# Optimization experiments

Measured on AMD Instinct MI355X. Metric: run time of the kernel, lower is better.

Reference implementation:

```python
import jax, jax.numpy as jnp
import numpy as np

B, N = 32, 200000          # images, flattened candidates per image (anchors*classes)
NUM_CLASSES = 21           # VOC-style class count for the label-offset trick
CONF_THR = 0.05            # cfg.PRED_CONF_THR
NMS_THR = 0.5              # cfg.PRED_NMS_THR
TOPK = 500                 # cfg.PRED_SELECT_TOPK
KEEP_MAX = 100             # cfg.PRED_NMS_KEEP


def setup_inputs() -> dict:
    key = jax.random.key(0)
    k1, k2, k3, k4 = jax.random.split(key, 4)
    pscores = jax.random.uniform(k1, (B, N), dtype=jnp.float32)
    # well-formed ltrb boxes in [0,1]: right>left, bottom>top
    xy1 = jax.random.uniform(k2, (B, N, 2), dtype=jnp.float32) * 0.8
    wh = jax.random.uniform(k3, (B, N, 2), dtype=jnp.float32) * 0.2 + 0.01
    pboxes = jnp.concatenate([xy1, xy1 + wh], axis=-1)
    plabels = jax.random.randint(k4, (B, N), 0, NUM_CLASSES)
    return {"pscores": pscores, "pboxes": pboxes, "plabels": plabels}


def _box_iou(a, b):
    # a: [K,4], b: [K,4] ltrb -> [K,K] pairwise IoU (torchvision convention)
    lt = jnp.maximum(a[:, None, :2], b[None, :, :2])
    rb = jnp.minimum(a[:, None, 2:], b[None, :, 2:])
    wh = jnp.clip(rb - lt, 0.0)
    inter = wh[..., 0] * wh[..., 1]
    area_a = (a[:, 2] - a[:, 0]) * (a[:, 3] - a[:, 1])
    area_b = (b[:, 2] - b[:, 0]) * (b[:, 3] - b[:, 1])
    return inter / (area_a[:, None] + area_b[None, :] - inter)


def _greedy_nms(iou_mat, valid, thr):
    # candidates are pre-sorted by score descending (lax.top_k output order)
    K = valid.shape[0]
    idxs = jnp.arange(K)

    def body(keep, i):
        suppressed = jnp.any(keep & (iou_mat[i] > thr) & (idxs < i))
        k = valid[i] & (~suppressed)
        return keep.at[i].set(k), None

    keep, _ = jax.lax.scan(body, jnp.zeros((K,), dtype=bool), idxs)
    return keep


def reference(pscores, pboxes, plabels):
    # ---- threshold + top-k pre-selection (mask_pos AND mask_topk) ----
    scores_k, idx = jax.lax.top_k(pscores, TOPK)          # [B,K] sorted desc
    valid = scores_k > CONF_THR                           # equivalent to mask_pos & mask_topk
    bidx = jnp.arange(B)[:, None]
    boxes_k = pboxes[bidx, idx]                           # [B,K,4]
    labels_k = plabels[bidx, idx]                         # [B,K]

    # ---- multi-class NMS via label offset trick (batched_nms) ----
    max_coord = jnp.max(jnp.where(valid[..., None], boxes_k, 0.0), axis=(1, 2))  # [B]
    offsets = labels_k.astype(boxes_k.dtype) * (max_coord[:, None] + 1.0)
    boxes_nms = boxes_k + offsets[..., None]              # [B,K,4]

    iou = jax.vmap(_box_iou)(boxes_nms, boxes_nms)        # [B,K,K]
    keep = jax.vmap(lambda m, v: _greedy_nms(m, v, NMS_THR))(iou, valid)  # [B,K] bool

    # ---- keep[:num_max] per batch ----
    rank = jnp.cumsum(keep.astype(jnp.int32), axis=1)
    keep = keep & (rank <= KEEP_MAX)

    # compact kept entries to front (jnp.argsort is stable -> score order preserved), pad to KEEP_MAX
    order = jnp.argsort(jnp.where(keep, 0, 1), axis=1)[:, :KEEP_MAX]       # [B,KEEP]
    out_valid = jnp.take_along_axis(keep, order, axis=1)                    # [B,KEEP]
    boxes2 = jnp.take_along_axis(boxes_k, order[..., None], axis=1) * out_valid[..., None]
    scores2 = jnp.take_along_axis(scores_k, order, axis=1) * out_valid
    labels2 = jnp.where(out_valid, jnp.take_along_axis(labels_k, order, axis=1), -1)
    ids_batch2 = jnp.where(out_valid, jnp.arange(B)[:, None], -1)
    return ids_batch2, boxes2, labels2, scores2, out_valid
```

## Files before the change

kernel.cpp:

```cpp
#include <hip/hip_runtime.h>
#include <stdint.h>

#pragma clang fp contract(off)

#define BB 32
#define NN 200000
#define N4 50000
#define KK 500
#define KEEPN 100
#define CAND_CAP 4096
#define CONF 0.05f
#define NMSTHR 0.5f
#define CNT_STRIDE 16
#define HBINS 16384
#define HSHIFT 18

typedef unsigned long long u64;


__device__ __forceinline__ unsigned int ordkey(float s) {
    unsigned int u = __float_as_uint(s);
    return (u & 0x80000000u) ? ~u : (u | 0x80000000u);
}

__global__ __launch_bounds__(512) void hist_kernel(const float4* __restrict__ ps4,
                                                   unsigned int* __restrict__ hist) {
    __shared__ unsigned int lh[HBINS];
    const int t = threadIdx.x;
    for (int i = t; i < HBINS; i += 512) lh[i] = 0;
    __syncthreads();
    const int b = blockIdx.y;
    const float4* p = ps4 + (size_t)b * N4;
    for (int i = blockIdx.x * 512 + t; i < N4; i += 8 * 512) {
        float4 v = p[i];
        atomicAdd(&lh[ordkey(v.x) >> HSHIFT], 1u);
        atomicAdd(&lh[ordkey(v.y) >> HSHIFT], 1u);
        atomicAdd(&lh[ordkey(v.z) >> HSHIFT], 1u);
        atomicAdd(&lh[ordkey(v.w) >> HSHIFT], 1u);
    }
    __syncthreads();
    unsigned int* hb = hist + (size_t)b * HBINS;
    for (int i = t; i < HBINS; i += 512) {
        unsigned int s = lh[i];
        if (s) atomicAdd(&hb[i], s);
    }
}

__global__ __launch_bounds__(1024) void scan_kernel(const unsigned int* __restrict__ hist,
                                                    unsigned int* __restrict__ p14arr,
                                                    unsigned int* __restrict__ cnt) {
    __shared__ unsigned int partial[1024];
    const int t = threadIdx.x, b = blockIdx.x;
    if (t == 0) cnt[b * CNT_STRIDE] = 0;
    const unsigned int* hb = hist + (size_t)b * HBINS;
    unsigned int v[16];
    unsigned int tot = 0;
    for (int j = 0; j < 16; ++j) { v[j] = hb[t * 16 + j]; tot += v[j]; }
    partial[t] = tot;
    __syncthreads();
    for (int d = 1; d < 1024; d <<= 1) {
        unsigned int add = (t + d < 1024) ? partial[t + d] : 0u;
        __syncthreads();
        partial[t] += add;
        __syncthreads();
    }
    unsigned int after = (t < 1023) ? partial[t + 1] : 0u;
    unsigned int sn = after;
    for (int j = 15; j >= 0; --j) {
        unsigned int s = sn + v[j];
        if (s >= (unsigned)KK && sn < (unsigned)KK) p14arr[b] = (unsigned)(t * 16 + j);
        sn = s;
    }
}

__global__ __launch_bounds__(256) void compact_kernel(const float4* __restrict__ ps4,
                                                      const unsigned int* __restrict__ p14arr,
                                                      u64* __restrict__ cand,
                                                      unsigned int* __restrict__ cnt) {
    __shared__ u64 sl[2048];
    __shared__ int lcnt;
    __shared__ unsigned int lbase;
    const int t = threadIdx.x;
    if (t == 0) lcnt = 0;
    __syncthreads();
    const int b = blockIdx.y;
    const unsigned int p14 = p14arr[b];
    const float4* p = ps4 + (size_t)b * N4;
    for (int k = 0; k < 2; ++k) {
        int i4 = blockIdx.x * 512 + k * 256 + t;
        if (i4 < N4) {
            float4 v = p[i4];
            int n = i4 << 2;
            unsigned int u;
            u = ordkey(v.x);
            if ((u >> HSHIFT) >= p14) { int pos = atomicAdd(&lcnt, 1);
                sl[pos] = ((u64)u << 32) | (unsigned int)(~(unsigned int)(n)); }
            u = ordkey(v.y);
            if ((u >> HSHIFT) >= p14) { int pos = atomicAdd(&lcnt, 1);
                sl[pos] = ((u64)u << 32) | (unsigned int)(~(unsigned int)(n + 1)); }
            u = ordkey(v.z);
            if ((u >> HSHIFT) >= p14) { int pos = atomicAdd(&lcnt, 1);
                sl[pos] = ((u64)u << 32) | (unsigned int)(~(unsigned int)(n + 2)); }
            u = ordkey(v.w);
            if ((u >> HSHIFT) >= p14) { int pos = atomicAdd(&lcnt, 1);
                sl[pos] = ((u64)u << 32) | (unsigned int)(~(unsigned int)(n + 3)); }
        }
    }
    __syncthreads();
    if (t == 0 && lcnt > 0) lbase = atomicAdd(&cnt[b * CNT_STRIDE], (unsigned)lcnt);
    __syncthreads();
    for (int i = t; i < lcnt; i += 256) {
        unsigned int pos = lbase + (unsigned)i;
        if (pos < CAND_CAP) cand[(size_t)b * CAND_CAP + pos] = sl[i];
    }
}

__global__ __launch_bounds__(1024) void final_kernel(const float* __restrict__ pboxes,
                                                     const int* __restrict__ plabels,
                                                     const u64* __restrict__ cand,
                                                     const unsigned int* __restrict__ cnt,
                                                     float* __restrict__ out) {
    __shared__ u64 kbuf[CAND_CAP];
    __shared__ u64 sel[1024];
    __shared__ float sboxes[KK][4];
    __shared__ float sshift[KK][4];
    __shared__ float sscore[KK];
    __shared__ int slabel[KK];
    __shared__ unsigned int h[256];
    __shared__ int clist[KK];
    __shared__ int ccnt[21], coff[22], cfill[21];
    __shared__ u64 validw[8];
    __shared__ int kept[KEEPN];
    __shared__ float wred[16];
    __shared__ u64 s_prefix;
    __shared__ unsigned int s_bin, s_region, s_cntgt;
    __shared__ int s_sc, s_nk;
    __shared__ float s_maxc;

    const int b = blockIdx.x;
    const int tid = threadIdx.x;
    const int lane = tid & 63;

    int m = (int)cnt[b * CNT_STRIDE];
    if (m > CAND_CAP) m = CAND_CAP;

    for (int i = tid; i < m; i += 1024)
        kbuf[i] = cand[(size_t)b * CAND_CAP + i];
    __syncthreads();

    u64 thr; int seln;
    if (m <= 1024) {
        thr = 0ULL; seln = m;
    } else {
        if (tid == 0) { s_prefix = 0ULL; s_cntgt = 0u; }
        __syncthreads();
        int shift = 56;
        for (; shift >= 0; shift -= 8) {
            if (tid < 256) h[tid] = 0u;
            __syncthreads();
            u64 pref = s_prefix;
            unsigned int cg = s_cntgt;
            for (int i = tid; i < m; i += 1024) {
                u64 k = kbuf[i];
                bool match = (shift == 56) || ((k >> (shift + 8)) == pref);
                if (match) atomicAdd(&h[(unsigned int)((k >> shift) & 0xFF)], 1u);
            }
            __syncthreads();
            for (int d = 1; d < 256; d <<= 1) {
                unsigned int add = (tid < 256 && tid + d < 256) ? h[tid + d] : 0u;
                __syncthreads();
                if (tid < 256) h[tid] += add;
                __syncthreads();
            }
            unsigned int target = (unsigned)KK - cg;
            if (tid < 256) {
                unsigned int st = h[tid];
                unsigned int stn = (tid < 255) ? h[tid + 1] : 0u;
                if (st >= target && stn < target) s_bin = (unsigned)tid;
            }
            __syncthreads();
            if (tid == 0) {
                unsigned int bin = s_bin;
                unsigned int sfx1 = (bin < 255) ? h[bin + 1] : 0u;
                s_region = h[bin] - sfx1;
                s_cntgt = cg + sfx1;
                s_prefix = (shift == 56) ? (u64)bin : ((pref << 8) | (u64)bin);
            }
            __syncthreads();
            if (s_cntgt + s_region <= 1024u) break;
        }
        thr = s_prefix << shift;
        seln = (int)(s_cntgt + s_region);
    }

    if (tid == 0) s_sc = 0;
    __syncthreads();
    for (int r = 0; r < 4; ++r) {
        int i = tid + r * 1024;
        u64 k = (i < m) ? kbuf[i] : 0ULL;
        bool p = (i < m) && (k >= thr);
        u64 mb = __ballot(p);
        int pre = __popcll(mb & ((1ULL << lane) - 1ULL));
        int tot = __popcll(mb);
        int base = 0;
        if (lane == 0 && tot > 0) base = atomicAdd(&s_sc, tot);
        base = __shfl(base, 0);
        if (p) sel[base + pre] = k;
    }
    __syncthreads();

    u64 myk = 0ULL; int myr = 0x7FFFFFFF;
    if (tid < seln) {
        myk = sel[tid];
        int r = 0;
        for (int j = 0; j < seln; ++j) r += (sel[j] > myk) ? 1 : 0;
        myr = r;
    }
    __syncthreads();
    if (tid < seln && myr < KK) sel[myr] = myk;
    __syncthreads();

    float sc = -1.0f;
    if (tid < KK) {
        u64 key = sel[tid];
        unsigned int lo = (unsigned int)key;
        unsigned int hi = (unsigned int)(key >> 32);
        int idx = (int)(~lo);
        unsigned int bits = (hi & 0x80000000u) ? (hi & 0x7FFFFFFFu) : ~hi;
        sc = __uint_as_float(bits);
        sscore[tid] = sc;
        const float4 bx = *(const float4*)(pboxes + (((size_t)b * NN + (size_t)idx) << 2));
        sboxes[tid][0] = bx.x; sboxes[tid][1] = bx.y;
        sboxes[tid][2] = bx.z; sboxes[tid][3] = bx.w;
        slabel[tid] = plabels[(size_t)b * NN + idx];
    }
    __syncthreads();

    bool v = (tid < KK) && (sc > CONF);
    u64 bm = __ballot(v);
    if (lane == 0 && (tid >> 6) < 8) validw[tid >> 6] = bm;
    float lm = 0.0f;
    if (v) lm = fmaxf(fmaxf(sboxes[tid][0], sboxes[tid][1]),
                      fmaxf(sboxes[tid][2], sboxes[tid][3]));
    for (int off = 32; off > 0; off >>= 1) lm = fmaxf(lm, __shfl_down(lm, off));
    if (lane == 0) wred[tid >> 6] = lm;
    __syncthreads();
    if (tid < 64) {
        float x = (tid < 16) ? wred[tid] : 0.0f;
        for (int off = 8; off > 0; off >>= 1) x = fmaxf(x, __shfl_down(x, off));
        if (tid == 0) s_maxc = x;
    }
    __syncthreads();

    if (tid < KK) {
        float off = (float)slabel[tid] * (s_maxc + 1.0f);
        sshift[tid][0] = sboxes[tid][0] + off;
        sshift[tid][1] = sboxes[tid][1] + off;
        sshift[tid][2] = sboxes[tid][2] + off;
        sshift[tid][3] = sboxes[tid][3] + off;
    }
    if (tid < 21) { ccnt[tid] = 0; cfill[tid] = 0; }
    __syncthreads();
    if (tid < KK) atomicAdd(&ccnt[slabel[tid]], 1);
    __syncthreads();
    if (tid == 0) {
        int acc = 0;
        for (int c = 0; c < 21; ++c) { coff[c] = acc; acc += ccnt[c]; }
        coff[21] = acc;
    }
    __syncthreads();
    if (tid < KK) {
        int c = slabel[tid];
        int pos = atomicAdd(&cfill[c], 1);
        clist[coff[c] + pos] = tid;
    }
    for (int i = tid; i < KK * 8; i += 1024) kbuf[i] = 0ULL;
    __syncthreads();

    if (tid < KK) {
        int c = slabel[tid];
        int n = ccnt[c], base = coff[c];
        float a0 = sshift[tid][0], a1 = sshift[tid][1],
              a2 = sshift[tid][2], a3 = sshift[tid][3];
        float areaA = (a2 - a0) * (a3 - a1);
        for (int q = 0; q < n; ++q) {
            int j = clist[base + q];
            float b0 = sshift[j][0], b1f = sshift[j][1],
                  b2f = sshift[j][2], b3f = sshift[j][3];
            float lt0 = fmaxf(a0, b0), lt1 = fmaxf(a1, b1f);
            float rb0 = fminf(a2, b2f), rb1 = fminf(a3, b3f);
            float ww = fmaxf(rb0 - lt0, 0.0f), hh = fmaxf(rb1 - lt1, 0.0f);
            float inter = ww * hh;
            float areaB = (b2f - b0) * (b3f - b1f);
            float iou = inter / (areaA + areaB - inter);
            if (iou > NMSTHR) kbuf[tid * 8 + (j >> 6)] |= (1ULL << (j & 63));
        }
    }
    __syncthreads();

    if (tid < 64) {
        u64 remv = 0ULL;
        u64 vw_reg = (lane < 8) ? validw[lane] : 0ULL;
        int nk = 0;
        for (int i = 0; i < KK && nk < KEEPN; ++i) {
            int w = i >> 6, bpos = i & 63;
            u64 rw = __shfl(remv, w);
            u64 vv = __shfl(vw_reg, w);
            bool alive = (((vv >> bpos) & 1ULL) != 0ULL) && (((rw >> bpos) & 1ULL) == 0ULL);
            if (alive) {
                if (lane == 0) kept[nk] = i;
                u64 roww = (lane < 8) ? kbuf[i * 8 + lane] : 0ULL;
                remv |= roww;
                nk++;
            }
        }
        if (lane == 0) s_nk = nk;
    }
    __syncthreads();

    if (tid < KEEPN) {
        const int O_BOX = BB * KEEPN;
        const int O_LAB = BB * KEEPN * 5;
        const int O_SCO = BB * KEEPN * 6;
        const int O_VAL = BB * KEEPN * 7;
        bool q = tid < s_nk;
        int i = q ? kept[tid] : 0;
        int g = b * KEEPN + tid;
        out[g]                 = q ? (float)b : -1.0f;
        out[O_BOX + g * 4 + 0] = q ? sboxes[i][0] : 0.0f;
        out[O_BOX + g * 4 + 1] = q ? sboxes[i][1] : 0.0f;
        out[O_BOX + g * 4 + 2] = q ? sboxes[i][2] : 0.0f;
        out[O_BOX + g * 4 + 3] = q ? sboxes[i][3] : 0.0f;
        out[O_LAB + g]         = q ? (float)slabel[i] : -1.0f;
        out[O_SCO + g]         = q ? sscore[i] : 0.0f;
        out[O_VAL + g]         = q ? 1.0f : 0.0f;
    }
}

extern "C" void kernel_launch(void* const* d_in, const int* in_sizes, int n_in,
                              void* d_out, int out_size, void* d_ws, size_t ws_size,
                              hipStream_t stream) {
    const float* pscores = (const float*)d_in[0];
    const float* pboxes  = (const float*)d_in[1];
    const int*   plabels = (const int*)d_in[2];
    float* out = (float*)d_out;

    uint8_t* ws = (uint8_t*)d_ws;
    unsigned int* hist = (unsigned int*)(ws + 0);
    unsigned int* cnt  = (unsigned int*)(ws + 2097152);
    unsigned int* p14  = (unsigned int*)(ws + 2099200);
    u64*          cand = (u64*)(ws + 2099328);

    hipMemsetAsync(hist, 0, 32 * HBINS * 4, stream);

    hist_kernel<<<dim3(8, BB), 512, 0, stream>>>((const float4*)pscores, hist);
    scan_kernel<<<BB, 1024, 0, stream>>>(hist, p14, cnt);
    compact_kernel<<<dim3((N4 + 511) / 512, BB), 256, 0, stream>>>(
        (const float4*)pscores, p14, cand, cnt);
    final_kernel<<<BB, 1024, 0, stream>>>(pboxes, plabels, cand, cnt, out);
}
```

Before: 229.6 us.

## Fuse histogram, compaction, selection and NMS into one per-image kernel

Replaces the four-kernel pipeline (global histogram, scan, compaction, final NMS) and the memset with a single kernel that runs one 1024-thread block per image. The histogram, threshold scan and candidate compaction now live in shared memory, removing global workspace traffic and extra launches. The radix-select scans now use wave shuffles, the rank sort uses readlane broadcasts, and the selection target is tightened. The per-class box shift is computed on the fly instead of being stored. The cost is that each image's 200k scores are read twice by a single block, so only 32 CUs stream the input.

```diff
diff --git a/kernel.cpp b/kernel.cpp
--- a/kernel.cpp
+++ b/kernel.cpp
@@ -11,213 +11,191 @@
 #define CAND_CAP 4096
 #define CONF 0.05f
 #define NMSTHR 0.5f
-#define CNT_STRIDE 16
+#define HSHIFT 18
 #define HBINS 16384
-#define HSHIFT 18
+#define SELTARGET 576
 
 typedef unsigned long long u64;
-
 
 __device__ __forceinline__ unsigned int ordkey(float s) {
     unsigned int u = __float_as_uint(s);
     return (u & 0x80000000u) ? ~u : (u | 0x80000000u);
 }
 
-__global__ __launch_bounds__(512) void hist_kernel(const float4* __restrict__ ps4,
-                                                   unsigned int* __restrict__ hist) {
-    __shared__ unsigned int lh[HBINS];
-    const int t = threadIdx.x;
-    for (int i = t; i < HBINS; i += 512) lh[i] = 0;
-    __syncthreads();
-    const int b = blockIdx.y;
-    const float4* p = ps4 + (size_t)b * N4;
-    for (int i = blockIdx.x * 512 + t; i < N4; i += 8 * 512) {
-        float4 v = p[i];
-        atomicAdd(&lh[ordkey(v.x) >> HSHIFT], 1u);
-        atomicAdd(&lh[ordkey(v.y) >> HSHIFT], 1u);
-        atomicAdd(&lh[ordkey(v.z) >> HSHIFT], 1u);
-        atomicAdd(&lh[ordkey(v.w) >> HSHIFT], 1u);
-    }
-    __syncthreads();
-    unsigned int* hb = hist + (size_t)b * HBINS;
-    for (int i = t; i < HBINS; i += 512) {
-        unsigned int s = lh[i];
-        if (s) atomicAdd(&hb[i], s);
-    }
-}
-
-__global__ __launch_bounds__(1024) void scan_kernel(const unsigned int* __restrict__ hist,
-                                                    unsigned int* __restrict__ p14arr,
-                                                    unsigned int* __restrict__ cnt) {
-    __shared__ unsigned int partial[1024];
-    const int t = threadIdx.x, b = blockIdx.x;
-    if (t == 0) cnt[b * CNT_STRIDE] = 0;
-    const unsigned int* hb = hist + (size_t)b * HBINS;
-    unsigned int v[16];
-    unsigned int tot = 0;
-    for (int j = 0; j < 16; ++j) { v[j] = hb[t * 16 + j]; tot += v[j]; }
-    partial[t] = tot;
-    __syncthreads();
-    for (int d = 1; d < 1024; d <<= 1) {
-        unsigned int add = (t + d < 1024) ? partial[t + d] : 0u;
-        __syncthreads();
-        partial[t] += add;
-        __syncthreads();
-    }
-    unsigned int after = (t < 1023) ? partial[t + 1] : 0u;
-    unsigned int sn = after;
-    for (int j = 15; j >= 0; --j) {
-        unsigned int s = sn + v[j];
-        if (s >= (unsigned)KK && sn < (unsigned)KK) p14arr[b] = (unsigned)(t * 16 + j);
-        sn = s;
-    }
-}
-
-__global__ __launch_bounds__(256) void compact_kernel(const float4* __restrict__ ps4,
-                                                      const unsigned int* __restrict__ p14arr,
-                                                      u64* __restrict__ cand,
-                                                      unsigned int* __restrict__ cnt) {
-    __shared__ u64 sl[2048];
-    __shared__ int lcnt;
-    __shared__ unsigned int lbase;
-    const int t = threadIdx.x;
-    if (t == 0) lcnt = 0;
-    __syncthreads();
-    const int b = blockIdx.y;
-    const unsigned int p14 = p14arr[b];
-    const float4* p = ps4 + (size_t)b * N4;
-    for (int k = 0; k < 2; ++k) {
-        int i4 = blockIdx.x * 512 + k * 256 + t;
-        if (i4 < N4) {
-            float4 v = p[i4];
-            int n = i4 << 2;
-            unsigned int u;
-            u = ordkey(v.x);
-            if ((u >> HSHIFT) >= p14) { int pos = atomicAdd(&lcnt, 1);
-                sl[pos] = ((u64)u << 32) | (unsigned int)(~(unsigned int)(n)); }
-            u = ordkey(v.y);
-            if ((u >> HSHIFT) >= p14) { int pos = atomicAdd(&lcnt, 1);
-                sl[pos] = ((u64)u << 32) | (unsigned int)(~(unsigned int)(n + 1)); }
-            u = ordkey(v.z);
-            if ((u >> HSHIFT) >= p14) { int pos = atomicAdd(&lcnt, 1);
-                sl[pos] = ((u64)u << 32) | (unsigned int)(~(unsigned int)(n + 2)); }
-            u = ordkey(v.w);
-            if ((u >> HSHIFT) >= p14) { int pos = atomicAdd(&lcnt, 1);
-                sl[pos] = ((u64)u << 32) | (unsigned int)(~(unsigned int)(n + 3)); }
-        }
-    }
-    __syncthreads();
-    if (t == 0 && lcnt > 0) lbase = atomicAdd(&cnt[b * CNT_STRIDE], (unsigned)lcnt);
-    __syncthreads();
-    for (int i = t; i < lcnt; i += 256) {
-        unsigned int pos = lbase + (unsigned)i;
-        if (pos < CAND_CAP) cand[(size_t)b * CAND_CAP + pos] = sl[i];
-    }
-}
-
-__global__ __launch_bounds__(1024) void final_kernel(const float* __restrict__ pboxes,
+__global__ __launch_bounds__(1024) void fused_kernel(const float4* __restrict__ ps4,
+                                                     const float* __restrict__ pboxes,
                                                      const int* __restrict__ plabels,
-                                                     const u64* __restrict__ cand,
-                                                     const unsigned int* __restrict__ cnt,
                                                      float* __restrict__ out) {
-    __shared__ u64 kbuf[CAND_CAP];
-    __shared__ u64 sel[1024];
-    __shared__ float sboxes[KK][4];
-    __shared__ float sshift[KK][4];
-    __shared__ float sscore[KK];
-    __shared__ int slabel[KK];
-    __shared__ unsigned int h[256];
-    __shared__ int clist[KK];
-    __shared__ int ccnt[21], coff[22], cfill[21];
-    __shared__ u64 validw[8];
-    __shared__ int kept[KEEPN];
-    __shared__ float wred[16];
-    __shared__ u64 s_prefix;
-    __shared__ unsigned int s_bin, s_region, s_cntgt;
-    __shared__ int s_sc, s_nk;
-    __shared__ float s_maxc;
+    __shared__ __align__(16) char smem[65536];
+    unsigned int* hist = (unsigned int*)smem;
+    u64*   kbuf   = (u64*)smem;
+    u64*   sel    = (u64*)(smem + 32768);
+    float* sboxes = (float*)(smem + 40960);
+    float* sscore = (float*)(smem + 48960);
+    int*   slabel = (int*)(smem + 50960);
+    int*   clist  = (int*)(smem + 52960);
+    unsigned int* h = (unsigned int*)(smem + 54960);
+    int* ccnt  = (int*)(smem + 55984);
+    int* coff  = (int*)(smem + 56068);
+    int* cfill = (int*)(smem + 56160);
+    u64* validw = (u64*)(smem + 56248);
+    int* kept   = (int*)(smem + 56312);
+    float* wred = (float*)(smem + 56712);
+    unsigned int* wsum = (unsigned int*)(smem + 57344);
+    u64* s_prefix = (u64*)(smem + 57472);
+    unsigned int* s_p14    = (unsigned int*)(smem + 57480);
+    int*          s_lcnt   = (int*)(smem + 57484);
+    int*          s_sc     = (int*)(smem + 57488);
+    unsigned int* s_region = (unsigned int*)(smem + 57492);
+    unsigned int* s_cntgt  = (unsigned int*)(smem + 57496);
+    int*          s_nk     = (int*)(smem + 57500);
+    float*        s_maxc   = (float*)(smem + 57504);
 
     const int b = blockIdx.x;
     const int tid = threadIdx.x;
     const int lane = tid & 63;
-
-    int m = (int)cnt[b * CNT_STRIDE];
+    const int wv = tid >> 6;
+
+    const float4* p = ps4 + (size_t)b * N4;
+
+    for (int i = tid; i < HBINS; i += 1024) hist[i] = 0;
+    __syncthreads();
+    for (int i = tid; i < N4; i += 1024) {
+        float4 v = p[i];
+        atomicAdd(&hist[ordkey(v.x) >> HSHIFT], 1u);
+        atomicAdd(&hist[ordkey(v.y) >> HSHIFT], 1u);
+        atomicAdd(&hist[ordkey(v.z) >> HSHIFT], 1u);
+        atomicAdd(&hist[ordkey(v.w) >> HSHIFT], 1u);
+    }
+    __syncthreads();
+
+    unsigned int v16[16];
+    unsigned int tot = 0;
+    for (int j = 0; j < 16; ++j) { v16[j] = hist[tid * 16 + j]; tot += v16[j]; }
+    __syncthreads();
+    unsigned int sfx = tot;
+    for (int off = 1; off < 64; off <<= 1) {
+        unsigned int t2 = __shfl_down(sfx, off);
+        sfx += (lane + off < 64) ? t2 : 0u;
+    }
+    if (lane == 0) wsum[wv] = sfx;
+    __syncthreads();
+    unsigned int wafter = 0;
+    for (int w2 = wv + 1; w2 < 16; ++w2) wafter += wsum[w2];
+    unsigned int after_me = wafter + (sfx - tot);
+    unsigned int sn = after_me;
+    for (int j = 15; j >= 0; --j) {
+        unsigned int s = sn + v16[j];
+        if (s >= (unsigned)KK && sn < (unsigned)KK) *s_p14 = (unsigned)(tid * 16 + j);
+        sn = s;
+    }
+    if (tid == 0) *s_lcnt = 0;
+    __syncthreads();
+
+    const unsigned int p14 = *s_p14;
+    for (int i = tid; i < N4; i += 1024) {
+        float4 v = p[i];
+        int n = i << 2;
+        unsigned int u;
+        u = ordkey(v.x);
+        if ((u >> HSHIFT) >= p14) { int pos = atomicAdd(s_lcnt, 1);
+            if (pos < CAND_CAP) kbuf[pos] = ((u64)u << 32) | (unsigned int)(~(unsigned int)(n)); }
+        u = ordkey(v.y);
+        if ((u >> HSHIFT) >= p14) { int pos = atomicAdd(s_lcnt, 1);
+            if (pos < CAND_CAP) kbuf[pos] = ((u64)u << 32) | (unsigned int)(~(unsigned int)(n + 1)); }
+        u = ordkey(v.z);
+        if ((u >> HSHIFT) >= p14) { int pos = atomicAdd(s_lcnt, 1);
+            if (pos < CAND_CAP) kbuf[pos] = ((u64)u << 32) | (unsigned int)(~(unsigned int)(n + 2)); }
+        u = ordkey(v.w);
+        if ((u >> HSHIFT) >= p14) { int pos = atomicAdd(s_lcnt, 1);
+            if (pos < CAND_CAP) kbuf[pos] = ((u64)u << 32) | (unsigned int)(~(unsigned int)(n + 3)); }
+    }
+    __syncthreads();
+    int m = *s_lcnt;
     if (m > CAND_CAP) m = CAND_CAP;
 
-    for (int i = tid; i < m; i += 1024)
-        kbuf[i] = cand[(size_t)b * CAND_CAP + i];
-    __syncthreads();
-
     u64 thr; int seln;
-    if (m <= 1024) {
+    int shift = 56;
+    if (m <= SELTARGET) {
         thr = 0ULL; seln = m;
     } else {
-        if (tid == 0) { s_prefix = 0ULL; s_cntgt = 0u; }
+        if (tid == 0) { *s_prefix = 0ULL; *s_cntgt = 0u; }
         __syncthreads();
-        int shift = 56;
         for (; shift >= 0; shift -= 8) {
             if (tid < 256) h[tid] = 0u;
             __syncthreads();
-            u64 pref = s_prefix;
-            unsigned int cg = s_cntgt;
+            u64 pref = *s_prefix;
+            unsigned int cg = *s_cntgt;
             for (int i = tid; i < m; i += 1024) {
                 u64 k = kbuf[i];
                 bool match = (shift == 56) || ((k >> (shift + 8)) == pref);
                 if (match) atomicAdd(&h[(unsigned int)((k >> shift) & 0xFF)], 1u);
             }
             __syncthreads();
-            for (int d = 1; d < 256; d <<= 1) {
-                unsigned int add = (tid < 256 && tid + d < 256) ? h[tid + d] : 0u;
-                __syncthreads();
-                if (tid < 256) h[tid] += add;
-                __syncthreads();
-            }
-            unsigned int target = (unsigned)KK - cg;
-            if (tid < 256) {
-                unsigned int st = h[tid];
-                unsigned int stn = (tid < 255) ? h[tid + 1] : 0u;
-                if (st >= target && stn < target) s_bin = (unsigned)tid;
+            if (wv == 0) {
+                unsigned int b4[4]; unsigned int lt = 0;
+                for (int j = 0; j < 4; ++j) { b4[j] = h[lane * 4 + j]; lt += b4[j]; }
+                unsigned int sx = lt;
+                for (int off = 1; off < 64; off <<= 1) {
+                    unsigned int t2 = __shfl_down(sx, off);
+                    sx += (lane + off < 64) ? t2 : 0u;
+                }
+                unsigned int after = sx - lt;
+                unsigned int target = (unsigned)KK - cg;
+                unsigned int sn2 = after;
+                for (int j = 3; j >= 0; --j) {
+                    unsigned int s = sn2 + b4[j];
+                    if (s >= target && sn2 < target) {
+                        unsigned int bin = (unsigned)(lane * 4 + j);
+                        *s_region = b4[j];
+                        *s_cntgt = cg + sn2;
+                        *s_prefix = (shift == 56) ? (u64)bin : ((pref << 8) | (u64)bin);
+                    }
+                    sn2 = s;
+                }
             }
             __syncthreads();
-            if (tid == 0) {
-                unsigned int bin = s_bin;
-                unsigned int sfx1 = (bin < 255) ? h[bin + 1] : 0u;
-                s_region = h[bin] - sfx1;
-                s_cntgt = cg + sfx1;
-                s_prefix = (shift == 56) ? (u64)bin : ((pref << 8) | (u64)bin);
+            if (*s_cntgt + *s_region <= (unsigned)SELTARGET) break;
+        }
+        if (shift < 0) shift = 0;
+        thr = (*s_prefix) << shift;
+        seln = (int)(*s_cntgt + *s_region);
+    }
+
+    if (tid == 0) *s_sc = 0;
+    __syncthreads();
+    for (int r0 = 0; r0 < 4; ++r0) {
+        int i = tid + r0 * 1024;
+        u64 k = (i < m) ? kbuf[i] : 0ULL;
+        bool pq = (i < m) && (k >= thr);
+        u64 mb = __ballot(pq);
+        int pre = __popcll(mb & ((1ULL << lane) - 1ULL));
+        int tt = __popcll(mb);
+        int base = 0;
+        if (lane == 0 && tt > 0) base = atomicAdd(s_sc, tt);
+        base = __shfl(base, 0);
+        if (pq) sel[base + pre] = k;
+    }
+    __syncthreads();
+
+    u64 myk = (tid < seln) ? sel[tid] : 0ULL;
+    int r = 0;
+    if ((tid & ~63) < seln) {
+        for (int base = 0; base < seln; base += 64) {
+            int i2 = base + lane;
+            u64 other = (i2 < seln) ? sel[i2] : 0ULL;
+            unsigned int olo = (unsigned int)other, ohi = (unsigned int)(other >> 32);
+            int lim = seln - base; if (lim > 64) lim = 64;
+            for (int t2 = 0; t2 < lim; ++t2) {
+                unsigned int blo = (unsigned int)__builtin_amdgcn_readlane((int)olo, t2);
+                unsigned int bhi = (unsigned int)__builtin_amdgcn_readlane((int)ohi, t2);
+                u64 o = ((u64)bhi << 32) | (u64)blo;
+                r += (o > myk) ? 1 : 0;
             }
-            __syncthreads();
-            if (s_cntgt + s_region <= 1024u) break;
         }
-        thr = s_prefix << shift;
-        seln = (int)(s_cntgt + s_region);
-    }
-
-    if (tid == 0) s_sc = 0;
-    __syncthreads();
-    for (int r = 0; r < 4; ++r) {
-        int i = tid + r * 1024;
-        u64 k = (i < m) ? kbuf[i] : 0ULL;
-        bool p = (i < m) && (k >= thr);
-        u64 mb = __ballot(p);
-        int pre = __popcll(mb & ((1ULL << lane) - 1ULL));
-        int tot = __popcll(mb);
-        int base = 0;
-        if (lane == 0 && tot > 0) base = atomicAdd(&s_sc, tot);
-        base = __shfl(base, 0);
-        if (p) sel[base + pre] = k;
-    }
-    __syncthreads();
-
-    u64 myk = 0ULL; int myr = 0x7FFFFFFF;
-    if (tid < seln) {
-        myk = sel[tid];
-        int r = 0;
-        for (int j = 0; j < seln; ++j) r += (sel[j] > myk) ? 1 : 0;
-        myr = r;
-    }
-    __syncthreads();
-    if (tid < seln && myr < KK) sel[myr] = myk;
+    }
+    __syncthreads();
+    if (tid < seln && r < KK) sel[r] = myk;
     __syncthreads();
 
     float sc = -1.0f;
@@ -230,34 +208,24 @@
         sc = __uint_as_float(bits);
         sscore[tid] = sc;
         const float4 bx = *(const float4*)(pboxes + (((size_t)b * NN + (size_t)idx) << 2));
-        sboxes[tid][0] = bx.x; sboxes[tid][1] = bx.y;
-        sboxes[tid][2] = bx.z; sboxes[tid][3] = bx.w;
+        sboxes[tid * 4 + 0] = bx.x; sboxes[tid * 4 + 1] = bx.y;
+        sboxes[tid * 4 + 2] = bx.z; sboxes[tid * 4 + 3] = bx.w;
         slabel[tid] = plabels[(size_t)b * NN + idx];
     }
     __syncthreads();
 
-    bool v = (tid < KK) && (sc > CONF);
-    u64 bm = __ballot(v);
-    if (lane == 0 && (tid >> 6) < 8) validw[tid >> 6] = bm;
-    float lm = 0.0f;
-    if (v) lm = fmaxf(fmaxf(sboxes[tid][0], sboxes[tid][1]),
-                      fmaxf(sboxes[tid][2], sboxes[tid][3]));
+    bool vq = (tid < KK) && (sc > CONF);
+    u64 bm = __ballot(vq);
+    if (lane == 0 && wv < 8) validw[wv] = bm;
+    float lm = vq ? fmaxf(fmaxf(sboxes[tid * 4 + 0], sboxes[tid * 4 + 1]),
+                          fmaxf(sboxes[tid * 4 + 2], sboxes[tid * 4 + 3])) : 0.0f;
     for (int off = 32; off > 0; off >>= 1) lm = fmaxf(lm, __shfl_down(lm, off));
-    if (lane == 0) wred[tid >> 6] = lm;
+    if (lane == 0) wred[wv] = lm;
     __syncthreads();
     if (tid < 64) {
         float x = (tid < 16) ? wred[tid] : 0.0f;
         for (int off = 8; off > 0; off >>= 1) x = fmaxf(x, __shfl_down(x, off));
-        if (tid == 0) s_maxc = x;
-    }
-    __syncthreads();
-
-    if (tid < KK) {
-        float off = (float)slabel[tid] * (s_maxc + 1.0f);
-        sshift[tid][0] = sboxes[tid][0] + off;
-        sshift[tid][1] = sboxes[tid][1] + off;
-        sshift[tid][2] = sboxes[tid][2] + off;
-        sshift[tid][3] = sboxes[tid][3] + off;
+        if (tid == 0) *s_maxc = x;
     }
     if (tid < 21) { ccnt[tid] = 0; cfill[tid] = 0; }
     __syncthreads();
@@ -277,16 +245,18 @@
     for (int i = tid; i < KK * 8; i += 1024) kbuf[i] = 0ULL;
     __syncthreads();
 
+    float ap1 = *s_maxc + 1.0f;
     if (tid < KK) {
         int c = slabel[tid];
-        int n = ccnt[c], base = coff[c];
-        float a0 = sshift[tid][0], a1 = sshift[tid][1],
-              a2 = sshift[tid][2], a3 = sshift[tid][3];
+        int n = ccnt[c], base0 = coff[c];
+        float aoff = (float)c * ap1;
+        float a0 = sboxes[tid * 4 + 0] + aoff, a1 = sboxes[tid * 4 + 1] + aoff;
+        float a2 = sboxes[tid * 4 + 2] + aoff, a3 = sboxes[tid * 4 + 3] + aoff;
         float areaA = (a2 - a0) * (a3 - a1);
         for (int q = 0; q < n; ++q) {
-            int j = clist[base + q];
-            float b0 = sshift[j][0], b1f = sshift[j][1],
-                  b2f = sshift[j][2], b3f = sshift[j][3];
+            int j = clist[base0 + q];
+            float b0 = sboxes[j * 4 + 0] + aoff, b1f = sboxes[j * 4 + 1] + aoff;
+            float b2f = sboxes[j * 4 + 2] + aoff, b3f = sboxes[j * 4 + 3] + aoff;
             float lt0 = fmaxf(a0, b0), lt1 = fmaxf(a1, b1f);
             float rb0 = fminf(a2, b2f), rb1 = fminf(a3, b3f);
             float ww = fmaxf(rb0 - lt0, 0.0f), hh = fmaxf(rb1 - lt1, 0.0f);
@@ -314,7 +284,7 @@
                 nk++;
             }
         }
-        if (lane == 0) s_nk = nk;
+        if (lane == 0) *s_nk = nk;
     }
     __syncthreads();
 
@@ -323,14 +293,14 @@
         const int O_LAB = BB * KEEPN * 5;
         const int O_SCO = BB * KEEPN * 6;
         const int O_VAL = BB * KEEPN * 7;
-        bool q = tid < s_nk;
+        bool q = tid < *s_nk;
         int i = q ? kept[tid] : 0;
         int g = b * KEEPN + tid;
         out[g]                 = q ? (float)b : -1.0f;
-        out[O_BOX + g * 4 + 0] = q ? sboxes[i][0] : 0.0f;
-        out[O_BOX + g * 4 + 1] = q ? sboxes[i][1] : 0.0f;
-        out[O_BOX + g * 4 + 2] = q ? sboxes[i][2] : 0.0f;
-        out[O_BOX + g * 4 + 3] = q ? sboxes[i][3] : 0.0f;
+        out[O_BOX + g * 4 + 0] = q ? sboxes[i * 4 + 0] : 0.0f;
+        out[O_BOX + g * 4 + 1] = q ? sboxes[i * 4 + 1] : 0.0f;
+        out[O_BOX + g * 4 + 2] = q ? sboxes[i * 4 + 2] : 0.0f;
+        out[O_BOX + g * 4 + 3] = q ? sboxes[i * 4 + 3] : 0.0f;
         out[O_LAB + g]         = q ? (float)slabel[i] : -1.0f;
         out[O_SCO + g]         = q ? sscore[i] : 0.0f;
         out[O_VAL + g]         = q ? 1.0f : 0.0f;
@@ -344,18 +314,5 @@
     const float* pboxes  = (const float*)d_in[1];
     const int*   plabels = (const int*)d_in[2];
     float* out = (float*)d_out;
-
-    uint8_t* ws = (uint8_t*)d_ws;
-    unsigned int* hist = (unsigned int*)(ws + 0);
-    unsigned int* cnt  = (unsigned int*)(ws + 2097152);
-    unsigned int* p14  = (unsigned int*)(ws + 2099200);
-    u64*          cand = (u64*)(ws + 2099328);
-
-    hipMemsetAsync(hist, 0, 32 * HBINS * 4, stream);
-
-    hist_kernel<<<dim3(8, BB), 512, 0, stream>>>((const float4*)pscores, hist);
-    scan_kernel<<<BB, 1024, 0, stream>>>(hist, p14, cnt);
-    compact_kernel<<<dim3((N4 + 511) / 512, BB), 256, 0, stream>>>(
-        (const float4*)pscores, p14, cand, cnt);
-    final_kernel<<<BB, 1024, 0, stream>>>(pboxes, plabels, cand, cnt, out);
+    fused_kernel<<<BB, 1024, 0, stream>>>((const float4*)pscores, pboxes, plabels, out);
 }
```

After: 266.7 us. 16.2% more time.
